# Optimization experiments

Hardware: AMD Instinct MI355X
Metric: run time of the kernel (lower is better)

The kernel has to match this reference:

```python
import jax, jax.numpy as jnp
import numpy as np

NUM_HEAD = 8


def setup_inputs() -> dict:
    key = jax.random.key(0)
    ks = jax.random.split(key, 9)
    B, T, Hz, N, H, Tc = 8, 48, 24, 1024, 512, 64
    return {
        "encoder_hidden": jax.random.normal(ks[0], (B, T, N, H), dtype=jnp.float32),
        "x_time": jax.random.normal(ks[1], (B, T, Tc), dtype=jnp.float32),
        "target_time": jax.random.normal(ks[2], (B, Hz, Tc), dtype=jnp.float32),
        "Wq": jax.random.normal(ks[3], (Tc, H), dtype=jnp.float32) * (Tc ** -0.5),
        "bq": jax.random.normal(ks[4], (H,), dtype=jnp.float32) * 0.02,
        "Wk": jax.random.normal(ks[5], (Tc, H), dtype=jnp.float32) * (Tc ** -0.5),
        "bk": jax.random.normal(ks[6], (H,), dtype=jnp.float32) * 0.02,
        "Wv": jax.random.normal(ks[7], (H, H), dtype=jnp.float32) * (H ** -0.5),
        "bv": jax.random.normal(ks[8], (H,), dtype=jnp.float32) * 0.02,
    }


def reference(encoder_hidden, x_time, target_time, Wq, bq, Wk, bk, Wv, bv):
    # encoder_hidden: [B, T, N, H]; x_time: [B, T, Tc]; target_time: [B, Hz, Tc]
    B, T, N, H = encoder_hidden.shape
    nh = NUM_HEAD
    d = H // nh
    Hz = target_time.shape[1]
    # Linear projections; split/cat over heads == reshape last dim to [nh, d]
    q = (target_time @ Wq + bq).reshape(B, Hz, nh, d)      # [B, Hz, nh, d]
    k = (x_time @ Wk + bk).reshape(B, T, nh, d)            # [B, T, nh, d]
    v = (encoder_hidden @ Wv + bv).reshape(B, T, N, nh, d)  # [B, T, N, nh, d]
    # Attention over time, shared across nodes
    scores = jnp.einsum('bihd,bjhd->bhij', q, k) / (d ** 0.5)  # [B, nh, Hz, T]
    attn = jax.nn.softmax(scores, axis=-1)
    # Broadcast attention across the node dimension
    X = jnp.einsum('bhij,bjnhd->binhd', attn, v)           # [B, Hz, N, nh, d]
    return X.reshape(B, Hz, N, H)                           # [B, Hz, N, H]
```

## Files before the change

### kernel.cpp

```cpp
#include <hip/hip_runtime.h>
#include <hip/hip_bf16.h>

#define Bb 8
#define Tt 48
#define HZ 24
#define Nn 1024
#define Hh 512
#define NHEAD 8

typedef short short8 __attribute__((ext_vector_type(8)));
typedef short bf16x4 __attribute__((ext_vector_type(4)));
typedef float f32x4 __attribute__((ext_vector_type(4)));

__device__ __forceinline__ ushort f2bf(float f) {
  uint u = __builtin_bit_cast(uint, f);
  u += 0x7FFFu + ((u >> 16) & 1u);
  return (ushort)(u >> 16);
}

__device__ __forceinline__ f32x4 mfma16(bf16x4 a, bf16x4 b, f32x4 c) {
#if __has_builtin(__builtin_amdgcn_mfma_f32_16x16x16bf16_1k)
  return __builtin_amdgcn_mfma_f32_16x16x16bf16_1k(a, b, c, 0, 0, 0);
#elif __has_builtin(__builtin_amdgcn_mfma_f32_16x16x16_bf16)
  return __builtin_amdgcn_mfma_f32_16x16x16_bf16(a, b, c, 0, 0, 0);
#else
  f32x4 d;
  asm volatile("v_mfma_f32_16x16x16_bf16 %0, %1, %2, %3\n\ts_nop 7\n\ts_nop 4"
               : "=v"(d) : "v"(a), "v"(b), "v"(c));
  return d;
#endif
}

__global__ void wvt2_kernel(const float* __restrict__ Wv, ushort* __restrict__ W2) {
  int t = blockIdx.x * 256 + threadIdx.x;
  int e = t & 7;
  int lane = (t >> 3) & 63;
  int f = (t >> 9) & 3;
  int kb = (t >> 11) & 7;
  int w = (t >> 14) & 3;
  int ch = t >> 16;
  int ki = f >> 1, nn = f & 1;
  int row = ch * 128 + w * 32 + nn * 16 + (lane & 15);
  int col = kb * 64 + ki * 32 + ((lane >> 4) << 3) + e;
  W2[t] = f2bf(Wv[col * 512 + row]);
}

__global__ void attn_kernel(const float* __restrict__ xt, const float* __restrict__ tt,
                            const float* __restrict__ Wq, const float* __restrict__ bq,
                            const float* __restrict__ Wk, const float* __restrict__ bk,
                            ushort* __restrict__ attnp) {
  __shared__ float qs[24][65];
  __shared__ float ks_[48][65];
  __shared__ float sc[24][49];
  int bh = blockIdx.x;
  int b = bh >> 3, h = bh & 7;
  int t = threadIdx.x;
  for (int e = t; e < 24 * 64; e += 256) {
    int i = e >> 6, dd = e & 63;
    float s = bq[h * 64 + dd];
    const float* r = tt + (b * 24 + i) * 64;
    #pragma unroll 8
    for (int c = 0; c < 64; ++c) s += r[c] * Wq[c * 512 + h * 64 + dd];
    qs[i][dd] = s;
  }
  for (int e = t; e < 48 * 64; e += 256) {
    int j = e >> 6, dd = e & 63;
    float s = bk[h * 64 + dd];
    const float* r = xt + (b * 48 + j) * 64;
    #pragma unroll 8
    for (int c = 0; c < 64; ++c) s += r[c] * Wk[c * 512 + h * 64 + dd];
    ks_[j][dd] = s;
  }
  __syncthreads();
  for (int e = t; e < 24 * 48; e += 256) {
    int i = e / 48, j = e - i * 48;
    float s = 0.f;
    #pragma unroll 8
    for (int dd = 0; dd < 64; ++dd) s += qs[i][dd] * ks_[j][dd];
    sc[i][j] = s * 0.125f;
  }
  __syncthreads();
  if (t < 32) {
    int i = t;
    ushort* orow = attnp + ((size_t)bh * 32 + i) * 64;
    if (i < 24) {
      float mx = -1e30f;
      for (int j = 0; j < 48; ++j) mx = fmaxf(mx, sc[i][j]);
      float sum = 0.f;
      for (int j = 0; j < 48; ++j) { float e = expf(sc[i][j] - mx); sc[i][j] = e; sum += e; }
      float inv = 1.f / sum;
      for (int j = 0; j < 48; ++j) orow[j] = f2bf(sc[i][j] * inv);
      for (int j = 48; j < 64; ++j) orow[j] = 0;
    } else {
      for (int j = 0; j < 64; ++j) orow[j] = 0;
    }
  }
}

#define A_BASE 0

__global__ __launch_bounds__(256, 3) void main_kernel(
    const float* __restrict__ EH, const ushort* __restrict__ W2,
    const ushort* __restrict__ attnp, const float* __restrict__ bv,
    float* __restrict__ out) {
  __shared__ __align__(128) char smem[49152];
  int bid = blockIdx.x;
  int b = bid >> 10, n = bid & 1023;
  int t = threadIdx.x;
  int lane = t & 63, w = t >> 6;
  int rowl = lane & 15;
  int colb = (lane >> 4) << 3;
  int colb16 = (lane >> 4) << 2;

  float bvr[4][2];
  #pragma unroll
  for (int c = 0; c < 4; ++c)
    #pragma unroll
    for (int nn = 0; nn < 2; ++nn)
      bvr[c][nn] = bv[c * 128 + w * 32 + nn * 16 + rowl];

  const ushort* wp0 = W2 + (size_t)w * 16384 + lane * 8;

  short8 bc[4], bn[4];
  #pragma unroll
  for (int f = 0; f < 4; ++f) bc[f] = *(const short8*)(wp0 + f * 512);

  {
    const float* ehb = EH + (((size_t)b * Tt) * Nn + n) * Hh;
    #pragma unroll 8
    for (int it = 0; it < 24; ++it) {
      int f = it * 256 + t;
      int j = f >> 7, c4 = f & 127;
      float4 v = *(const float4*)(ehb + (size_t)j * (Nn * Hh) + c4 * 4);
      uint2 p;
      p.x = (uint)f2bf(v.x) | ((uint)f2bf(v.y) << 16);
      p.y = (uint)f2bf(v.z) | ((uint)f2bf(v.w) << 16);
      int off = (j << 10) + (c4 << 3);
      off ^= (j & 7) << 4;
      *(uint2*)(smem + A_BASE + off) = p;
    }
  }
  __syncthreads();

  #pragma unroll
  for (int ch = 0; ch < 4; ++ch) {
    const ushort* wp = W2 + (size_t)(ch * 4 + w) * 16384 + lane * 8;
    f32x4 acc[3][2] = {};
    #pragma unroll
    for (int kb = 0; kb < 8; ++kb) {
      if (kb < 7) {
        #pragma unroll
        for (int f = 0; f < 4; ++f)
          bn[f] = *(const short8*)(wp + (kb + 1) * 2048 + f * 512);
      } else if (ch < 3) {
        #pragma unroll
        for (int f = 0; f < 4; ++f)
          bn[f] = *(const short8*)(wp + 65536 + f * 512);
      }
      #pragma unroll
      for (int ki = 0; ki < 2; ++ki) {
        short8 af[3];
        int kc = kb * 64 + ki * 32 + colb;
        #pragma unroll
        for (int m = 0; m < 3; ++m) {
          int j = m * 16 + rowl;
          int off = (j << 10) + (kc << 1);
          off ^= (j & 7) << 4;
          af[m] = *(const short8*)(smem + A_BASE + off);
        }
        #pragma unroll
        for (int m = 0; m < 3; ++m) {
          acc[m][0] = __builtin_amdgcn_mfma_f32_16x16x32_bf16(af[m], bc[ki * 2 + 0], acc[m][0], 0, 0, 0);
          acc[m][1] = __builtin_amdgcn_mfma_f32_16x16x32_bf16(af[m], bc[ki * 2 + 1], acc[m][1], 0, 0, 0);
        }
      }
      #pragma unroll
      for (int f = 0; f < 4; ++f) bc[f] = bn[f];
    }

    int h = 2 * ch + (w >> 1);
    const ushort* arow = attnp + ((size_t)(b * 8 + h) * 32) * 64;
    f32x4 x[2][2] = {};
    #pragma unroll
    for (int m = 0; m < 3; ++m) {
      bf16x4 pa[2];
      #pragma unroll
      for (int itl = 0; itl < 2; ++itl)
        pa[itl] = *(const bf16x4*)(arow + (itl * 16 + rowl) * 64 + m * 16 + colb16);
      #pragma unroll
      for (int nn = 0; nn < 2; ++nn) {
        bf16x4 vbq;
        vbq[0] = (short)f2bf(acc[m][nn][0]);
        vbq[1] = (short)f2bf(acc[m][nn][1]);
        vbq[2] = (short)f2bf(acc[m][nn][2]);
        vbq[3] = (short)f2bf(acc[m][nn][3]);
        x[0][nn] = mfma16(pa[0], vbq, x[0][nn]);
        x[1][nn] = mfma16(pa[1], vbq, x[1][nn]);
      }
    }

    #pragma unroll
    for (int itl = 0; itl < 2; ++itl) {
      int ib = itl * 16 + ((lane >> 4) << 2);
      #pragma unroll
      for (int nn = 0; nn < 2; ++nn) {
        int hd = ch * 128 + w * 32 + nn * 16 + rowl;
        float bvv = bvr[ch][nn];
        #pragma unroll
        for (int r = 0; r < 4; ++r) {
          int i = ib + r;
          if (i < 24)
            out[(((size_t)b * HZ + i) * Nn + n) * Hh + hd] = x[itl][nn][r] + bvv;
        }
      }
    }
  }
}

extern "C" void kernel_launch(void* const* d_in, const int* in_sizes, int n_in,
                              void* d_out, int out_size, void* d_ws, size_t ws_size,
                              hipStream_t stream) {
  (void)in_sizes; (void)n_in; (void)out_size; (void)ws_size;
  const float* EH = (const float*)d_in[0];
  const float* xt = (const float*)d_in[1];
  const float* tt = (const float*)d_in[2];
  const float* Wq = (const float*)d_in[3];
  const float* bq = (const float*)d_in[4];
  const float* Wk = (const float*)d_in[5];
  const float* bk = (const float*)d_in[6];
  const float* Wv = (const float*)d_in[7];
  const float* bv = (const float*)d_in[8];
  float* out = (float*)d_out;
  ushort* W2 = (ushort*)d_ws;
  ushort* attnp = (ushort*)((char*)d_ws + 512 * 1024);

  wvt2_kernel<<<1024, 256, 0, stream>>>(Wv, W2);
  attn_kernel<<<64, 256, 0, stream>>>(xt, tt, Wq, bq, Wk, bk, attnp);
  main_kernel<<<8192, 256, 0, stream>>>(EH, W2, attnp, bv, out);
}
```

Measured before the change: 484.5 us.

## Flatten chunk loop and deepen W prefetch to two stages with MFMA priority

Merges the nested chunk/k-block loops into one 32-step loop and keeps two stages of Wv fragments in registers, so each weight load is issued two steps ahead of use. LDS fragments for both k-halves are loaded before the MFMA burst, and s_setprio raises wave priority while the MFMAs issue. Launch bounds drop from 3 to 2 blocks per SM to make room for the extra registers, which lowers occupancy and the latency hiding that came with it.

```diff
diff --git a/kernel.cpp b/kernel.cpp
--- a/kernel.cpp
+++ b/kernel.cpp
@@ -99,7 +99,7 @@
 
 #define A_BASE 0
 
-__global__ __launch_bounds__(256, 3) void main_kernel(
+__global__ __launch_bounds__(256, 2) void main_kernel(
     const float* __restrict__ EH, const ushort* __restrict__ W2,
     const ushort* __restrict__ attnp, const float* __restrict__ bv,
     float* __restrict__ out) {
@@ -119,11 +119,13 @@
     for (int nn = 0; nn < 2; ++nn)
       bvr[c][nn] = bv[c * 128 + w * 32 + nn * 16 + rowl];
 
-  const ushort* wp0 = W2 + (size_t)w * 16384 + lane * 8;
-
-  short8 bc[4], bn[4];
-  #pragma unroll
-  for (int f = 0; f < 4; ++f) bc[f] = *(const short8*)(wp0 + f * 512);
+  const ushort* wbase = W2 + (size_t)w * 16384 + lane * 8;
+
+  short8 b0[4], b1[4];
+  #pragma unroll
+  for (int f = 0; f < 4; ++f) b0[f] = *(const short8*)(wbase + f * 512);
+  #pragma unroll
+  for (int f = 0; f < 4; ++f) b1[f] = *(const short8*)(wbase + 2048 + f * 512);
 
   {
     const float* ehb = EH + (((size_t)b * Tt) * Nn + n) * Hh;
@@ -142,77 +144,90 @@
   }
   __syncthreads();
 
-  #pragma unroll
-  for (int ch = 0; ch < 4; ++ch) {
-    const ushort* wp = W2 + (size_t)(ch * 4 + w) * 16384 + lane * 8;
-    f32x4 acc[3][2] = {};
-    #pragma unroll
-    for (int kb = 0; kb < 8; ++kb) {
-      if (kb < 7) {
-        #pragma unroll
-        for (int f = 0; f < 4; ++f)
-          bn[f] = *(const short8*)(wp + (kb + 1) * 2048 + f * 512);
-      } else if (ch < 3) {
-        #pragma unroll
-        for (int f = 0; f < 4; ++f)
-          bn[f] = *(const short8*)(wp + 65536 + f * 512);
+  f32x4 acc[3][2] = {};
+  #pragma unroll
+  for (int ck = 0; ck < 32; ++ck) {
+    const int kb = ck & 7;
+    short8 bnext[4];
+    if (ck < 30) {
+      const int ck2 = ck + 2;
+      const ushort* wp2 = wbase + (size_t)((ck2 >> 3) * 4) * 16384 + (ck2 & 7) * 2048;
+      #pragma unroll
+      for (int f = 0; f < 4; ++f) bnext[f] = *(const short8*)(wp2 + f * 512);
+    }
+    short8 af[2][3];
+    #pragma unroll
+    for (int ki = 0; ki < 2; ++ki) {
+      int kc = kb * 64 + ki * 32 + colb;
+      #pragma unroll
+      for (int m = 0; m < 3; ++m) {
+        int j = m * 16 + rowl;
+        int off = (j << 10) + (kc << 1);
+        off ^= (j & 7) << 4;
+        af[ki][m] = *(const short8*)(smem + A_BASE + off);
       }
-      #pragma unroll
-      for (int ki = 0; ki < 2; ++ki) {
-        short8 af[3];
-        int kc = kb * 64 + ki * 32 + colb;
-        #pragma unroll
-        for (int m = 0; m < 3; ++m) {
-          int j = m * 16 + rowl;
-          int off = (j << 10) + (kc << 1);
-          off ^= (j & 7) << 4;
-          af[m] = *(const short8*)(smem + A_BASE + off);
-        }
-        #pragma unroll
-        for (int m = 0; m < 3; ++m) {
-          acc[m][0] = __builtin_amdgcn_mfma_f32_16x16x32_bf16(af[m], bc[ki * 2 + 0], acc[m][0], 0, 0, 0);
-          acc[m][1] = __builtin_amdgcn_mfma_f32_16x16x32_bf16(af[m], bc[ki * 2 + 1], acc[m][1], 0, 0, 0);
+    }
+    __builtin_amdgcn_s_setprio(1);
+    #pragma unroll
+    for (int m = 0; m < 3; ++m) {
+      acc[m][0] = __builtin_amdgcn_mfma_f32_16x16x32_bf16(af[0][m], b0[0], acc[m][0], 0, 0, 0);
+      acc[m][1] = __builtin_amdgcn_mfma_f32_16x16x32_bf16(af[0][m], b0[1], acc[m][1], 0, 0, 0);
+    }
+    #pragma unroll
+    for (int m = 0; m < 3; ++m) {
+      acc[m][0] = __builtin_amdgcn_mfma_f32_16x16x32_bf16(af[1][m], b0[2], acc[m][0], 0, 0, 0);
+      acc[m][1] = __builtin_amdgcn_mfma_f32_16x16x32_bf16(af[1][m], b0[3], acc[m][1], 0, 0, 0);
+    }
+    __builtin_amdgcn_s_setprio(0);
+    #pragma unroll
+    for (int f = 0; f < 4; ++f) b0[f] = b1[f];
+    if (ck < 30) {
+      #pragma unroll
+      for (int f = 0; f < 4; ++f) b1[f] = bnext[f];
+    }
+
+    if (kb == 7) {
+      const int ch = ck >> 3;
+      int h = 2 * ch + (w >> 1);
+      const ushort* arow = attnp + ((size_t)(b * 8 + h) * 32) * 64;
+      f32x4 x[2][2] = {};
+      #pragma unroll
+      for (int m = 0; m < 3; ++m) {
+        bf16x4 pa[2];
+        #pragma unroll
+        for (int itl = 0; itl < 2; ++itl)
+          pa[itl] = *(const bf16x4*)(arow + (itl * 16 + rowl) * 64 + m * 16 + colb16);
+        #pragma unroll
+        for (int nn = 0; nn < 2; ++nn) {
+          bf16x4 vbq;
+          vbq[0] = (short)f2bf(acc[m][nn][0]);
+          vbq[1] = (short)f2bf(acc[m][nn][1]);
+          vbq[2] = (short)f2bf(acc[m][nn][2]);
+          vbq[3] = (short)f2bf(acc[m][nn][3]);
+          x[0][nn] = mfma16(pa[0], vbq, x[0][nn]);
+          x[1][nn] = mfma16(pa[1], vbq, x[1][nn]);
         }
       }
       #pragma unroll
-      for (int f = 0; f < 4; ++f) bc[f] = bn[f];
-    }
-
-    int h = 2 * ch + (w >> 1);
-    const ushort* arow = attnp + ((size_t)(b * 8 + h) * 32) * 64;
-    f32x4 x[2][2] = {};
-    #pragma unroll
-    for (int m = 0; m < 3; ++m) {
-      bf16x4 pa[2];
-      #pragma unroll
-      for (int itl = 0; itl < 2; ++itl)
-        pa[itl] = *(const bf16x4*)(arow + (itl * 16 + rowl) * 64 + m * 16 + colb16);
-      #pragma unroll
-      for (int nn = 0; nn < 2; ++nn) {
-        bf16x4 vbq;
-        vbq[0] = (short)f2bf(acc[m][nn][0]);
-        vbq[1] = (short)f2bf(acc[m][nn][1]);
-        vbq[2] = (short)f2bf(acc[m][nn][2]);
-        vbq[3] = (short)f2bf(acc[m][nn][3]);
-        x[0][nn] = mfma16(pa[0], vbq, x[0][nn]);
-        x[1][nn] = mfma16(pa[1], vbq, x[1][nn]);
-      }
-    }
-
-    #pragma unroll
-    for (int itl = 0; itl < 2; ++itl) {
-      int ib = itl * 16 + ((lane >> 4) << 2);
-      #pragma unroll
-      for (int nn = 0; nn < 2; ++nn) {
-        int hd = ch * 128 + w * 32 + nn * 16 + rowl;
-        float bvv = bvr[ch][nn];
-        #pragma unroll
-        for (int r = 0; r < 4; ++r) {
-          int i = ib + r;
-          if (i < 24)
-            out[(((size_t)b * HZ + i) * Nn + n) * Hh + hd] = x[itl][nn][r] + bvv;
+      for (int itl = 0; itl < 2; ++itl) {
+        int ib = itl * 16 + ((lane >> 4) << 2);
+        #pragma unroll
+        for (int nn = 0; nn < 2; ++nn) {
+          int hd = ch * 128 + w * 32 + nn * 16 + rowl;
+          float bvv = bvr[ch][nn];
+          #pragma unroll
+          for (int r = 0; r < 4; ++r) {
+            int i = ib + r;
+            if (i < 24)
+              out[(((size_t)b * HZ + i) * Nn + n) * Hh + hd] = x[itl][nn][r] + bvv;
+          }
         }
       }
+      #pragma unroll
+      for (int m = 0; m < 3; ++m)
+        #pragma unroll
+        for (int nn = 0; nn < 2; ++nn)
+          acc[m][nn] = f32x4{0.f, 0.f, 0.f, 0.f};
     }
   }
 }
```

Result: faster. 471.4 us (-2.7%).
